# Kernel optimization log

Measured on AMD Instinct MI355X. Metric: run time of the kernel, lower is better.

Reference implementation:

```python
import jax, jax.numpy as jnp
import numpy as np

N = 8192       # number of graph nodes (A.shape[0])
D_IN = 256     # input_dim
D_THETA = 256  # hard-coded theta projection dim
D_OUT = 256    # output_dim
K = 5          # per-row top-k sparsification
BN_EPS = 1e-5
LRELU_SLOPE = 0.01


def setup_inputs() -> dict:
    key = jax.random.key(0)
    k0, k1, k2 = jax.random.split(key, 3)
    H = jax.random.normal(k0, (N, D_IN), dtype=jnp.float32)
    # Linear(input_dim, 256)
    W_theta = jax.random.normal(k1, (D_IN, D_THETA), dtype=jnp.float32) * (1.0 / np.sqrt(D_IN))
    b_theta = jnp.zeros((D_THETA,), dtype=jnp.float32)
    # Linear(input_dim, output_dim)
    W_out = jax.random.normal(k2, (D_IN, D_OUT), dtype=jnp.float32) * (1.0 / np.sqrt(D_IN))
    b_out = jnp.zeros((D_OUT,), dtype=jnp.float32)
    # BatchNorm1d(input_dim) affine params (fresh init)
    bn_gamma = jnp.ones((D_IN,), dtype=jnp.float32)
    bn_beta = jnp.zeros((D_IN,), dtype=jnp.float32)
    return {"H": H, "bn_gamma": bn_gamma, "bn_beta": bn_beta,
            "W_theta": W_theta, "b_theta": b_theta,
            "W_out": W_out, "b_out": b_out}


def reference(H, bn_gamma, bn_beta, W_theta, b_theta, W_out, b_out):
    # BatchNorm1d in training mode: biased batch stats over the node axis
    mu = H.mean(axis=0)
    var = H.var(axis=0)  # biased, matching torch normalization
    Hn = (H - mu) * jax.lax.rsqrt(var + BN_EPS) * bn_gamma + bn_beta  # [N, D_IN]

    # theta projection -> SAM affinity
    Hx = Hn @ W_theta + b_theta                                        # [N, D_THETA]
    nrm = jnp.maximum(jnp.linalg.norm(Hx, axis=1, keepdims=True), 1e-12)  # F.normalize eps
    F1 = Hx / nrm
    dist = jnp.clip(F1 @ F1.T, -1.0, 1.0)                              # [N, N]
    sam = jnp.nan_to_num(jnp.arccos(dist))
    # original SAM() detaches (numpy round-trip): affinity is a constant wrt grads
    sam = jax.lax.stop_gradient(sam)

    A = jnp.maximum(jax.nn.sigmoid(jnp.exp(-0.2 * sam)), 0.1)          # clamp(min=0.1)

    # per-row top-k sparsification (fused replacement of the python double loop)
    _, idx = jax.lax.top_k(A, K)                                       # [N, K]
    mask = jnp.zeros_like(A).at[jnp.arange(N)[:, None], idx].set(1.0)
    A = A * mask

    # D^{-1/2} A D^{-1/2} without materializing diag matrices
    dinv = A.sum(axis=1) ** -0.5                                       # [N]
    A_hat = dinv[:, None] * A * dinv[None, :]

    out = A_hat @ (Hn @ W_out + b_out)                                 # [N, D_OUT]
    out = jnp.where(out >= 0, out, LRELU_SLOPE * out)                  # LeakyReLU
    return out, A
```

## Files before the change

### kernel.cpp

```cpp
#include <hip/hip_runtime.h>
#include <hip/hip_bf16.h>
#include <cstdint>
#include <cstddef>

#define NN 8192
#define DD 256

using bf16 = __hip_bfloat16;
typedef unsigned short ushort_t;
typedef unsigned int uint32;
typedef short short8 __attribute__((ext_vector_type(8)));
typedef float f32x4 __attribute__((ext_vector_type(4)));

#define GL2LDS(g, l) __builtin_amdgcn_global_load_lds( \
  (const __attribute__((address_space(1))) void*)(g),  \
  (__attribute__((address_space(3))) void*)(l), 16, 0, 0)

__device__ __forceinline__ float ldin(const void* p, int flag, size_t i) {
  return flag ? __bfloat162float(((const bf16*)p)[i]) : ((const float*)p)[i];
}

__device__ __forceinline__ void ins8(float v, int jj, float (&lv)[8], int (&li)[8]) {
  if (v <= lv[7]) return;
  int cnt = 0;
#pragma unroll
  for (int s = 0; s < 8; ++s) cnt += (lv[s] >= v) ? 1 : 0;
#pragma unroll
  for (int s = 7; s >= 1; --s) {
    bool sh = (s > cnt);
    lv[s] = sh ? lv[s-1] : lv[s];
    li[s] = sh ? li[s-1] : li[s];
  }
#pragma unroll
  for (int s = 0; s < 8; ++s) if (s == cnt) { lv[s] = v; li[s] = jj; }
}

__device__ __forceinline__ void ins8t(float v, int jj, float (&lv)[8], int (&li)[8]) {
  bool lose = (lv[7] > v) || (lv[7] == v && li[7] < jj);
  if (lose) return;
  int cnt = 0;
#pragma unroll
  for (int s = 0; s < 8; ++s) cnt += ((lv[s] > v) || (lv[s] == v && li[s] < jj)) ? 1 : 0;
#pragma unroll
  for (int s = 7; s >= 1; --s) {
    bool sh = (s > cnt);
    lv[s] = sh ? lv[s-1] : lv[s];
    li[s] = sh ? li[s-1] : li[s];
  }
#pragma unroll
  for (int s = 0; s < 8; ++s) if (s == cnt) { lv[s] = v; li[s] = jj; }
}

__device__ __forceinline__ bool lexgt(float va, int ia, float vb, int ib) {
  return (va > vb) || (va == vb && ia < ib);
}

__global__ void k_detect(const ushort_t* __restrict__ Hu, int* __restrict__ flag) {
  __shared__ int cnt;
  if (threadIdx.x == 0) cnt = 0;
  __syncthreads();
  int sane = 0;
  for (int u = 0; u < 16; ++u) {
    int idx = 2 * (threadIdx.x * 16 + u);
    ushort_t h = Hu[idx];
    int e = (h >> 7) & 0xFF;
    sane += (e >= 113 && e <= 133) ? 1 : 0;
  }
  atomicAdd(&cnt, sane);
  __syncthreads();
  if (threadIdx.x == 0) *flag = (cnt > 2048) ? 1 : 0;
}

__global__ void k_transposeH(const void* __restrict__ H, const int* __restrict__ pflag,
                             float* __restrict__ HT) {
  int flag = *pflag;
  __shared__ float tile[64][65];
  int i0 = blockIdx.x * 64;
  int c0 = blockIdx.y * 64;
  int tid = threadIdx.x;
  int r = tid >> 2, cb = (tid & 3) * 16;
#pragma unroll
  for (int u = 0; u < 16; ++u)
    tile[r][cb + u] = ldin(H, flag, (size_t)(i0 + r) * DD + c0 + cb + u);
  __syncthreads();
  int c = tid >> 2, rb = (tid & 3) * 16;
#pragma unroll
  for (int u4 = 0; u4 < 4; ++u4) {
    float4 t;
    t.x = tile[rb + 4*u4 + 0][c];
    t.y = tile[rb + 4*u4 + 1][c];
    t.z = tile[rb + 4*u4 + 2][c];
    t.w = tile[rb + 4*u4 + 3][c];
    *(float4*)&HT[(size_t)(c0 + c) * NN + i0 + rb + 4*u4] = t;
  }
}

__global__ __launch_bounds__(256) void k_statsT(const float* __restrict__ HT,
                                                float* __restrict__ mu32, float* __restrict__ rs32) {
  __shared__ float buf[8192];
  int c = blockIdx.x;
  int tid = threadIdx.x;
#pragma unroll
  for (int it = 0; it < 8; ++it) {
    int idx = it * 1024 + tid * 4;
    *(float4*)&buf[idx] = *(const float4*)&HT[(size_t)c * NN + idx];
  }
  __syncthreads();
  if (tid == 0) {
    float acc = 0.0f;
    for (int r = 0; r < 8192; r += 32) {
      float4 v[8];
#pragma unroll
      for (int q = 0; q < 8; ++q) v[q] = *(const float4*)&buf[r + q * 4];
#pragma unroll
      for (int q = 0; q < 8; ++q) {
        acc = __fadd_rn(acc, v[q].x);
        acc = __fadd_rn(acc, v[q].y);
        acc = __fadd_rn(acc, v[q].z);
        acc = __fadd_rn(acc, v[q].w);
      }
    }
    float mu = __fdiv_rn(acc, 8192.0f);
    float vacc = 0.0f;
    for (int r = 0; r < 8192; r += 32) {
      float4 v[8];
#pragma unroll
      for (int q = 0; q < 8; ++q) v[q] = *(const float4*)&buf[r + q * 4];
#pragma unroll
      for (int q = 0; q < 8; ++q) {
        float d0 = __fsub_rn(v[q].x, mu); vacc = __fadd_rn(vacc, __fmul_rn(d0, d0));
        float d1 = __fsub_rn(v[q].y, mu); vacc = __fadd_rn(vacc, __fmul_rn(d1, d1));
        float d2 = __fsub_rn(v[q].z, mu); vacc = __fadd_rn(vacc, __fmul_rn(d2, d2));
        float d3 = __fsub_rn(v[q].w, mu); vacc = __fadd_rn(vacc, __fmul_rn(d3, d3));
      }
    }
    float var = __fdiv_rn(vacc, 8192.0f);
    mu32[c] = mu;
    rs32[c] = __fdiv_rn(1.0f, sqrtf(__fadd_rn(var, 1e-5f)));
  }
}

__global__ __launch_bounds__(256) void k_hxn(const void* __restrict__ H,
    const int* __restrict__ pflag, const float* __restrict__ mu32, const float* __restrict__ rs32,
    const void* __restrict__ gamma, const void* __restrict__ beta,
    const void* __restrict__ Wt, const void* __restrict__ bt,
    float* __restrict__ Hn, float* __restrict__ F1,
    ushort_t* __restrict__ F1hi, ushort_t* __restrict__ F1lo) {
  int flag = *pflag;
  __shared__ float sHn[8][256];
  __shared__ float sHx[8][256];
  __shared__ float sp[8][16];
  __shared__ float snrm[8];
  const int r0 = blockIdx.x * 8;
  const int n = threadIdx.x;
  float g  = ldin(gamma, flag, n);
  float b  = ldin(beta, flag, n);
  float mu = mu32[n], rs = rs32[n];
#pragma unroll
  for (int r = 0; r < 8; ++r) {
    float t = __fsub_rn(ldin(H, flag, (size_t)(r0 + r) * DD + n), mu);
    t = __fmul_rn(t, rs);
    t = __fmul_rn(t, g);
    t = __fadd_rn(t, b);
    sHn[r][n] = t;
    Hn[(size_t)(r0 + r) * DD + n] = t;
  }
  __syncthreads();
  float acc[8];
#pragma unroll
  for (int r = 0; r < 8; ++r) acc[r] = 0.0f;
#pragma unroll 8
  for (int k = 0; k < DD; ++k) {
    float w = ldin(Wt, flag, (size_t)k * DD + n);
#pragma unroll
    for (int r = 0; r < 8; ++r) acc[r] = fmaf(sHn[r][k], w, acc[r]);
  }
  float btn = ldin(bt, flag, n);
#pragma unroll
  for (int r = 0; r < 8; ++r) sHx[r][n] = __fadd_rn(acc[r], btn);
  __syncthreads();
  if (n < 128) {
    int r = n >> 4, s = n & 15;
    int base = (s >> 3) * 128 + (s & 7);
    float e0 = sHx[r][base];
    float part = __fmul_rn(e0, e0);
#pragma unroll
    for (int t = 1; t < 16; ++t) {
      float e = sHx[r][base + 8 * t];
      part = __fadd_rn(part, __fmul_rn(e, e));
    }
    sp[r][s] = part;
  }
  __syncthreads();
  if (n < 8) {
    const float* p = sp[n];
    float P1 = __fadd_rn(__fadd_rn(__fadd_rn(p[0], p[1]), __fadd_rn(p[2], p[3])),
                         __fadd_rn(__fadd_rn(p[4], p[5]), __fadd_rn(p[6], p[7])));
    float P2 = __fadd_rn(__fadd_rn(__fadd_rn(p[8], p[9]), __fadd_rn(p[10], p[11])),
                         __fadd_rn(__fadd_rn(p[12], p[13]), __fadd_rn(p[14], p[15])));
    snrm[n] = fmaxf(sqrtf(__fadd_rn(P1, P2)), 1e-12f);
  }
  __syncthreads();
#pragma unroll
  for (int r = 0; r < 8; ++r) {
    float xn = __fdiv_rn(sHx[r][n], snrm[r]);
    size_t idx = (size_t)(r0 + r) * DD + n;
    F1[idx] = xn;
    bf16 hi = __float2bfloat16(xn);
    float lo = __fsub_rn(xn, __bfloat162float(hi));
    F1hi[idx] = *(ushort_t*)&hi;
    bf16 lob = __float2bfloat16(lo);
    F1lo[idx] = *(ushort_t*)&lob;
  }
}

__global__ __launch_bounds__(256) void k_gemm_s(
    const ushort_t* __restrict__ F1hi, const ushort_t* __restrict__ F1lo,
    int jc, float* __restrict__ S) {
  __shared__ __align__(16) ushort_t AH[4096];
  __shared__ __align__(16) ushort_t AL[4096];
  __shared__ __align__(16) ushort_t BH[4096];
  __shared__ __align__(16) ushort_t BL[4096];
  const int tid = threadIdx.x;
  const int w = tid >> 6, lane = tid & 63;
  const int quad = lane >> 4, l15 = lane & 15;
  const int wi = w >> 1, wj = w & 1;
  const int i0 = blockIdx.y * 128;
  const int j0loc = blockIdx.x * 128;
  const int j0 = jc * 2048 + j0loc;

  const int rofs = lane >> 2;
  const int ccl  = (lane & 3) ^ (rofs & 3);
  const int laneElem = rofs * DD + ccl * 8;

  f32x4 acc[4][4];
#pragma unroll
  for (int fr = 0; fr < 4; ++fr)
#pragma unroll
    for (int fc = 0; fc < 4; ++fc) acc[fr][fc] = (f32x4)0.0f;

  for (int chunk = 0; chunk < 8; ++chunk) {
    const int kofs = chunk * 32;
    __syncthreads();
#pragma unroll
    for (int q = 0; q < 2; ++q) {
      const int s = w * 2 + q;
      const size_t ga = (size_t)(i0 + s * 16) * DD + kofs;
      const size_t gb = (size_t)(j0 + s * 16) * DD + kofs;
      GL2LDS(F1hi + ga + laneElem, &AH[s * 512]);
      GL2LDS(F1lo + ga + laneElem, &AL[s * 512]);
      GL2LDS(F1hi + gb + laneElem, &BH[s * 512]);
      GL2LDS(F1lo + gb + laneElem, &BL[s * 512]);
    }
    __syncthreads();
    short8 ah[4], al[4], bh[4], bl[4];
#pragma unroll
    for (int fr = 0; fr < 4; ++fr) {
      int row = wi * 64 + fr * 16 + l15;
      int g = quad ^ (row & 3);
      ah[fr] = *(const short8*)&AH[row * 32 + g * 8];
      al[fr] = *(const short8*)&AL[row * 32 + g * 8];
    }
#pragma unroll
    for (int fc = 0; fc < 4; ++fc) {
      int row = wj * 64 + fc * 16 + l15;
      int g = quad ^ (row & 3);
      bh[fc] = *(const short8*)&BH[row * 32 + g * 8];
      bl[fc] = *(const short8*)&BL[row * 32 + g * 8];
    }
#pragma unroll
    for (int fr = 0; fr < 4; ++fr)
#pragma unroll
      for (int fc = 0; fc < 4; ++fc) {
        acc[fr][fc] = __builtin_amdgcn_mfma_f32_16x16x32_bf16(ah[fr], bh[fc], acc[fr][fc], 0, 0, 0);
        acc[fr][fc] = __builtin_amdgcn_mfma_f32_16x16x32_bf16(ah[fr], bl[fc], acc[fr][fc], 0, 0, 0);
        acc[fr][fc] = __builtin_amdgcn_mfma_f32_16x16x32_bf16(al[fr], bh[fc], acc[fr][fc], 0, 0, 0);
      }
  }
#pragma unroll
  for (int fr = 0; fr < 4; ++fr) {
#pragma unroll
    for (int reg = 0; reg < 4; ++reg) {
      int row = i0 + wi * 64 + fr * 16 + quad * 4 + reg;
#pragma unroll
      for (int fc = 0; fc < 4; ++fc) {
        int coll = j0loc + wj * 64 + fc * 16 + l15;
        S[(size_t)row * 2048 + coll] = acc[fr][fc][reg];
      }
    }
  }
}

__global__ __launch_bounds__(256) void k_scan(const float* __restrict__ S, int jc,
                                              float* __restrict__ candv, int* __restrict__ candi) {
  int w = threadIdx.x >> 6, lane = threadIdx.x & 63;
  int row = blockIdx.x * 4 + w;
  const int jbase = jc * 2048;
  float lv[8]; int li[8];
#pragma unroll
  for (int e = 0; e < 8; ++e) { lv[e] = -3.0e38f; li[e] = 0x7fffffff; }
  const float* p = S + (size_t)row * 2048;
#pragma unroll
  for (int it = 0; it < 8; ++it) {
    int col = it * 256 + lane * 4;
    float4 v = *(const float4*)&p[col];
    float m4 = fmaxf(fmaxf(v.x, v.y), fmaxf(v.z, v.w));
    if (m4 > lv[7]) {
      ins8(v.x, jbase + col + 0, lv, li);
      ins8(v.y, jbase + col + 1, lv, li);
      ins8(v.z, jbase + col + 2, lv, li);
      ins8(v.w, jbase + col + 3, lv, li);
    }
  }
#pragma unroll
  for (int m = 1; m <= 32; m <<= 1) {
    float bv[8]; int bi[8];
#pragma unroll
    for (int e = 0; e < 8; ++e) {
      bv[e] = __shfl_xor(lv[e], m, 64);
      bi[e] = __shfl_xor(li[e], m, 64);
    }
#pragma unroll
    for (int e = 0; e < 8; ++e) {
      bool t = lexgt(lv[e], li[e], bv[7 - e], bi[7 - e]);
      lv[e] = t ? lv[e] : bv[7 - e];
      li[e] = t ? li[e] : bi[7 - e];
    }
#pragma unroll
    for (int d = 4; d >= 1; d >>= 1) {
#pragma unroll
      for (int e = 0; e < 8; ++e) {
        if ((e & d) == 0) {
          int f = e + d;
          bool sw = lexgt(lv[f], li[f], lv[e], li[e]);
          float tv = lv[e]; int ti = li[e];
          lv[e] = sw ? lv[f] : lv[e];  li[e] = sw ? li[f] : li[e];
          lv[f] = sw ? tv : lv[f];     li[f] = sw ? ti : li[f];
        }
      }
    }
  }
  if (lane == 0) {
    size_t base = ((size_t)row * 4 + jc) * 8;
#pragma unroll
    for (int e = 0; e < 8; ++e) { candv[base + e] = lv[e]; candi[base + e] = li[e]; }
  }
}

__global__ void k_merge(const float* __restrict__ candv, const int* __restrict__ candi,
                        int* __restrict__ cand8) {
  int row = blockIdx.x * 256 + threadIdx.x;
  float bv[8]; int bj[8];
#pragma unroll
  for (int e = 0; e < 8; ++e) { bv[e] = -3.0e38f; bj[e] = 0x7fffffff; }
  for (int t = 0; t < 32; ++t) {
    float v = candv[(size_t)row * 32 + t];
    int j   = candi[(size_t)row * 32 + t];
    ins8t(v, j, bv, bj);
  }
#pragma unroll
  for (int e = 0; e < 8; ++e) cand8[row * 8 + e] = bj[e];
}

__global__ void k_rerank(const float* __restrict__ F1, const int* __restrict__ cand8,
                         int* __restrict__ top5i, float* __restrict__ top5v,
                         float* __restrict__ dinv) {
  int w = threadIdx.x >> 6, lane = threadIdx.x & 63;
  int row = blockIdx.x * 4 + w;
  int jl = 0x7fffffff;
  float a32 = -1.0f;
  if (lane < 8) {
    jl = cand8[row * 8 + lane];
    const float* xi = F1 + (size_t)row * DD;
    const float* xj = F1 + (size_t)jl * DD;
    float acc = 0.0f;
#pragma unroll 8
    for (int k = 0; k < DD; ++k)
      acc = fmaf(xi[k], xj[k], acc);
    float d = fminf(fmaxf(acc, -1.0f), 1.0f);
    float sam = acosf(d);
    float xx = expf(__fmul_rn(-0.2f, sam));
    float sig = __fdiv_rn(1.0f, __fadd_rn(1.0f, expf(-xx)));
    a32 = fmaxf(sig, 0.1f);
  }
  float av[8]; int aj[8];
#pragma unroll
  for (int l = 0; l < 8; ++l) { av[l] = __shfl(a32, l, 64); aj[l] = __shfl(jl, l, 64); }
  if (lane == 0) {
    bool used[8] = {false,false,false,false,false,false,false,false};
    double dsum = 0.0;
#pragma unroll
    for (int k = 0; k < 5; ++k) {
      float bv = -2.0f; int bj = 0x7fffffff; int bs = -1;
#pragma unroll
      for (int s = 0; s < 8; ++s) {
        bool better = (!used[s]) && ((av[s] > bv) || (av[s] == bv && aj[s] < bj));
        bs = better ? s : bs;
        bv = better ? av[s] : bv;
        bj = better ? aj[s] : bj;
      }
#pragma unroll
      for (int s = 0; s < 8; ++s) used[s] = used[s] || (s == bs);
      top5i[row * 5 + k] = bj;
      top5v[row * 5 + k] = bv;
      dsum += (double)bv;
    }
    dinv[row] = (float)(1.0 / sqrt(dsum));
  }
}

__global__ __launch_bounds__(256) void k_zout(const float* __restrict__ Hn,
    const int* __restrict__ top5i, const float* __restrict__ top5v,
    const float* __restrict__ dinv, const void* __restrict__ Wo,
    const void* __restrict__ bo, const int* __restrict__ pflag, void* __restrict__ outp) {
  int flag = *pflag;
  __shared__ float sZ[8][256];
  __shared__ float ssr[8];
  const int r0 = blockIdx.x * 8;
  const int n = threadIdx.x;
#pragma unroll
  for (int r = 0; r < 8; ++r) {
    int i = r0 + r;
    float di = dinv[i];
    double z = 0.0;
    float sr = 0.0f;
#pragma unroll
    for (int k = 0; k < 5; ++k) {
      int j = top5i[i * 5 + k];
      float wgt = di * top5v[i * 5 + k] * dinv[j];
      z += (double)wgt * (double)Hn[(size_t)j * DD + n];
      sr += wgt;
    }
    sZ[r][n] = (float)z;
    if (n == 0) ssr[r] = sr;
  }
  __syncthreads();
  float acc[8];
#pragma unroll
  for (int r = 0; r < 8; ++r) acc[r] = 0.0f;
#pragma unroll 8
  for (int k = 0; k < DD; ++k) {
    float w = ldin(Wo, flag, (size_t)k * DD + n);
#pragma unroll
    for (int r = 0; r < 8; ++r) acc[r] = fmaf(sZ[r][k], w, acc[r]);
  }
  float bon = ldin(bo, flag, n);
#pragma unroll
  for (int r = 0; r < 8; ++r) {
    float v = acc[r] + ssr[r] * bon;
    v = (v >= 0.0f) ? v : 0.01f * v;
    size_t idx = (size_t)(r0 + r) * DD + n;
    if (flag) ((bf16*)outp)[idx] = __float2bfloat16(v);
    else      ((float*)outp)[idx] = v;
  }
}

__global__ __launch_bounds__(256) void k_zeroscatter(void* __restrict__ d_out,
    const int* __restrict__ pflag, const int* __restrict__ top5i,
    const float* __restrict__ top5v) {
  int flag = *pflag;
  size_t esize = flag ? 2 : 4;
  int r0 = blockIdx.x * 2;
  char* Abase = (char*)d_out + (size_t)NN * DD * esize;
  uint4* rowp = (uint4*)(Abase + (size_t)r0 * NN * esize);
  int nvec = (int)((2 * (size_t)NN * esize) >> 4);
  uint4 z; z.x = 0; z.y = 0; z.z = 0; z.w = 0;
  for (int i = threadIdx.x; i < nvec; i += 256) rowp[i] = z;
  __syncthreads();
  int t = threadIdx.x;
  if (t < 10) {
    int r = r0 + t / 5, k = t % 5;
    int col = top5i[r * 5 + k];
    float v = top5v[r * 5 + k];
    if (flag) ((bf16*)Abase)[(size_t)r * NN + col] = __float2bfloat16(v);
    else      ((float*)Abase)[(size_t)r * NN + col] = v;
  }
}

extern "C" void kernel_launch(void* const* d_in, const int* in_sizes, int n_in,
                              void* d_out, int out_size, void* d_ws, size_t ws_size,
                              hipStream_t stream) {
  (void)in_sizes; (void)n_in; (void)out_size; (void)ws_size;
  const void* H     = d_in[0];
  const void* gamma = d_in[1];
  const void* beta  = d_in[2];
  const void* Wt    = d_in[3];
  const void* bt    = d_in[4];
  const void* Wo    = d_in[5];
  const void* bo    = d_in[6];

  const size_t MB = 1048576;
  char* zb = (char*)d_out + 8 * MB;
  float*    Hn32  = (float*)(zb + 0);
  float*    F1_32 = (float*)(zb + 8 * MB);
  ushort_t* F1hi  = (ushort_t*)(zb + 16 * MB);
  ushort_t* F1lo  = (ushort_t*)(zb + 20 * MB);
  float*    candv = (float*)(zb + 24 * MB);
  int*      candi = (int*)(zb + 25 * MB);
  float*    HT    = (float*)(zb + 36 * MB);
  float*    mu32  = (float*)(zb + 44 * MB);
  float*    rs32  = (float*)(zb + 44 * MB + 4096);
  int*      cand8 = (int*)(zb + 44 * MB + 8192);
  float*    dinv  = (float*)(zb + 44 * MB + 270336);
  float*    Schunk= (float*)(zb + 48 * MB);

  char* ws = (char*)d_ws;
  int*   flag  = (int*)(ws + 0);
  int*   top5i = (int*)(ws + 256);
  float* top5v = (float*)(ws + 164096);

  k_detect<<<dim3(1), dim3(256), 0, stream>>>((const ushort_t*)H, flag);
  k_transposeH<<<dim3(128, 4), dim3(256), 0, stream>>>(H, flag, HT);
  k_statsT<<<dim3(256), dim3(256), 0, stream>>>(HT, mu32, rs32);
  k_hxn<<<dim3(1024), dim3(256), 0, stream>>>(H, flag, mu32, rs32, gamma, beta,
                                              Wt, bt, Hn32, F1_32, F1hi, F1lo);
  for (int jc = 0; jc < 4; ++jc) {
    k_gemm_s<<<dim3(16, 64), dim3(256), 0, stream>>>(F1hi, F1lo, jc, Schunk);
    k_scan<<<dim3(2048), dim3(256), 0, stream>>>(Schunk, jc, candv, candi);
  }
  k_merge<<<dim3(32), dim3(256), 0, stream>>>(candv, candi, cand8);
  k_rerank<<<dim3(2048), dim3(256), 0, stream>>>(F1_32, cand8, top5i, top5v, dinv);
  k_zout<<<dim3(1024), dim3(256), 0, stream>>>(Hn32, top5i, top5v, dinv, Wo, bo, flag, d_out);
  k_zeroscatter<<<dim3(4096), dim3(256), 0, stream>>>(d_out, flag, top5i, top5v);
}
```

Measured before the change: 838.4 us.

## Exploit Gram symmetry and fuse top-k candidate selection into the similarity GEMM

Computes only the lower-triangular 128x128 tiles of F1·F1ᵀ, using a triangular block index, and applies each tile to both its rows and the transposed columns. Per-tile top-8 candidates are extracted directly from the MFMA accumulators with sorting networks and shuffle merges, so the full similarity chunk is no longer written to and re-read from global memory. The per-chunk scan kernel is removed. k_merge becomes wave-parallel over 128 candidate lists per row. In exchange, the GEMM epilogue is heavier and there is a larger 64MB candidate buffer to write and merge.

New measurement: 1.071 ms. 1.28x slower.

```diff
diff --git a/kernel.cpp b/kernel.cpp
--- a/kernel.cpp
+++ b/kernel.cpp
@@ -2,6 +2,7 @@
 #include <hip/hip_bf16.h>
 #include <cstdint>
 #include <cstddef>
+#include <cmath>
 
 #define NN 8192
 #define DD 256
@@ -35,24 +36,43 @@
   for (int s = 0; s < 8; ++s) if (s == cnt) { lv[s] = v; li[s] = jj; }
 }
 
-__device__ __forceinline__ void ins8t(float v, int jj, float (&lv)[8], int (&li)[8]) {
-  bool lose = (lv[7] > v) || (lv[7] == v && li[7] < jj);
-  if (lose) return;
-  int cnt = 0;
-#pragma unroll
-  for (int s = 0; s < 8; ++s) cnt += ((lv[s] > v) || (lv[s] == v && li[s] < jj)) ? 1 : 0;
-#pragma unroll
-  for (int s = 7; s >= 1; --s) {
-    bool sh = (s > cnt);
-    lv[s] = sh ? lv[s-1] : lv[s];
-    li[s] = sh ? li[s-1] : li[s];
-  }
-#pragma unroll
-  for (int s = 0; s < 8; ++s) if (s == cnt) { lv[s] = v; li[s] = jj; }
-}
-
 __device__ __forceinline__ bool lexgt(float va, int ia, float vb, int ib) {
   return (va > vb) || (va == vb && ia < ib);
+}
+
+__device__ __forceinline__ void bimerge(float (&lv)[8], int (&li)[8], int m) {
+  float bv[8]; int bi[8];
+#pragma unroll
+  for (int e = 0; e < 8; ++e) {
+    bv[e] = __shfl_xor(lv[e], m, 64);
+    bi[e] = __shfl_xor(li[e], m, 64);
+  }
+#pragma unroll
+  for (int e = 0; e < 8; ++e) {
+    bool t = lexgt(lv[e], li[e], bv[7 - e], bi[7 - e]);
+    lv[e] = t ? lv[e] : bv[7 - e];
+    li[e] = t ? li[e] : bi[7 - e];
+  }
+#pragma unroll
+  for (int d = 4; d >= 1; d >>= 1) {
+#pragma unroll
+    for (int e = 0; e < 8; ++e) {
+      if ((e & d) == 0) {
+        int f = e + d;
+        bool sw = lexgt(lv[f], li[f], lv[e], li[e]);
+        float tv = lv[e]; int ti = li[e];
+        lv[e] = sw ? lv[f] : lv[e];  li[e] = sw ? li[f] : li[e];
+        lv[f] = sw ? tv : lv[f];     li[f] = sw ? ti : li[f];
+      }
+    }
+  }
+}
+
+__device__ __forceinline__ void cswap(float& va, int& ia, float& vb, int& ib) {
+  bool sw = lexgt(vb, ib, va, ia);
+  float tv = va; int ti = ia;
+  va = sw ? vb : va; ia = sw ? ib : ia;
+  vb = sw ? tv : vb; ib = sw ? ti : ib;
 }
 
 __global__ void k_detect(const ushort_t* __restrict__ Hu, int* __restrict__ flag) {
@@ -214,20 +234,25 @@
   }
 }
 
-__global__ __launch_bounds__(256) void k_gemm_s(
+__global__ __launch_bounds__(256) void k_gemm_sym(
     const ushort_t* __restrict__ F1hi, const ushort_t* __restrict__ F1lo,
-    int jc, float* __restrict__ S) {
+    float* __restrict__ candv, int* __restrict__ candi) {
   __shared__ __align__(16) ushort_t AH[4096];
   __shared__ __align__(16) ushort_t AL[4096];
   __shared__ __align__(16) ushort_t BH[4096];
   __shared__ __align__(16) ushort_t BL[4096];
+  const int bidx = blockIdx.x;
+  int it = (int)((sqrt(8.0 * (double)bidx + 1.0) - 1.0) * 0.5);
+  while ((it + 1) * (it + 2) / 2 <= bidx) ++it;
+  while (it * (it + 1) / 2 > bidx) --it;
+  const int jt = bidx - it * (it + 1) / 2;
+
   const int tid = threadIdx.x;
   const int w = tid >> 6, lane = tid & 63;
   const int quad = lane >> 4, l15 = lane & 15;
   const int wi = w >> 1, wj = w & 1;
-  const int i0 = blockIdx.y * 128;
-  const int j0loc = blockIdx.x * 128;
-  const int j0 = jc * 2048 + j0loc;
+  const int i0 = it * 128;
+  const int j0 = jt * 128;
 
   const int rofs = lane >> 2;
   const int ccl  = (lane & 3) ^ (rofs & 3);
@@ -277,89 +302,86 @@
         acc[fr][fc] = __builtin_amdgcn_mfma_f32_16x16x32_bf16(al[fr], bh[fc], acc[fr][fc], 0, 0, 0);
       }
   }
+
 #pragma unroll
   for (int fr = 0; fr < 4; ++fr) {
 #pragma unroll
     for (int reg = 0; reg < 4; ++reg) {
-      int row = i0 + wi * 64 + fr * 16 + quad * 4 + reg;
+      float sv[4]; int sj[4];
 #pragma unroll
       for (int fc = 0; fc < 4; ++fc) {
-        int coll = j0loc + wj * 64 + fc * 16 + l15;
-        S[(size_t)row * 2048 + coll] = acc[fr][fc][reg];
-      }
-    }
-  }
-}
-
-__global__ __launch_bounds__(256) void k_scan(const float* __restrict__ S, int jc,
-                                              float* __restrict__ candv, int* __restrict__ candi) {
+        sv[fc] = acc[fr][fc][reg];
+        sj[fc] = j0 + wj * 64 + fc * 16 + l15;
+      }
+      cswap(sv[0], sj[0], sv[1], sj[1]);
+      cswap(sv[2], sj[2], sv[3], sj[3]);
+      cswap(sv[0], sj[0], sv[2], sj[2]);
+      cswap(sv[1], sj[1], sv[3], sj[3]);
+      cswap(sv[1], sj[1], sv[2], sj[2]);
+      float lv[8]; int li[8];
+#pragma unroll
+      for (int e = 0; e < 4; ++e) { lv[e] = sv[e]; li[e] = sj[e]; }
+#pragma unroll
+      for (int e = 4; e < 8; ++e) { lv[e] = -3.0e38f; li[e] = 0x7fffffff; }
+      bimerge(lv, li, 1);
+      bimerge(lv, li, 2);
+      bimerge(lv, li, 4);
+      bimerge(lv, li, 8);
+      int rowg = i0 + wi * 64 + fr * 16 + quad * 4 + reg;
+      if (l15 < 8) {
+        size_t base = ((size_t)rowg * 128 + 2 * jt + wj) * 8;
+        candv[base + l15] = lv[l15];
+        candi[base + l15] = li[l15];
+      }
+    }
+  }
+  if (it != jt) {
+#pragma unroll
+    for (int fc = 0; fc < 4; ++fc) {
+      float lv[8]; int li[8];
+#pragma unroll
+      for (int e = 0; e < 8; ++e) { lv[e] = -3.0e38f; li[e] = 0x7fffffff; }
+#pragma unroll
+      for (int fr = 0; fr < 4; ++fr)
+#pragma unroll
+        for (int reg = 0; reg < 4; ++reg)
+          ins8(acc[fr][fc][reg], i0 + wi * 64 + fr * 16 + quad * 4 + reg, lv, li);
+      bimerge(lv, li, 16);
+      bimerge(lv, li, 32);
+      int jg = j0 + wj * 64 + fc * 16 + l15;
+      size_t base = ((size_t)jg * 128 + 2 * it + wi) * 8;
+#pragma unroll
+      for (int e = 0; e < 2; ++e) {
+        candv[base + quad * 2 + e] = lv[quad * 2 + e];
+        candi[base + quad * 2 + e] = li[quad * 2 + e];
+      }
+    }
+  }
+}
+
+__global__ __launch_bounds__(256) void k_merge(const float* __restrict__ candv,
+                                               const int* __restrict__ candi,
+                                               int* __restrict__ cand8) {
   int w = threadIdx.x >> 6, lane = threadIdx.x & 63;
   int row = blockIdx.x * 4 + w;
-  const int jbase = jc * 2048;
   float lv[8]; int li[8];
 #pragma unroll
   for (int e = 0; e < 8; ++e) { lv[e] = -3.0e38f; li[e] = 0x7fffffff; }
-  const float* p = S + (size_t)row * 2048;
-#pragma unroll
-  for (int it = 0; it < 8; ++it) {
-    int col = it * 256 + lane * 4;
-    float4 v = *(const float4*)&p[col];
-    float m4 = fmaxf(fmaxf(v.x, v.y), fmaxf(v.z, v.w));
-    if (m4 > lv[7]) {
-      ins8(v.x, jbase + col + 0, lv, li);
-      ins8(v.y, jbase + col + 1, lv, li);
-      ins8(v.z, jbase + col + 2, lv, li);
-      ins8(v.w, jbase + col + 3, lv, li);
-    }
-  }
-#pragma unroll
-  for (int m = 1; m <= 32; m <<= 1) {
-    float bv[8]; int bi[8];
-#pragma unroll
-    for (int e = 0; e < 8; ++e) {
-      bv[e] = __shfl_xor(lv[e], m, 64);
-      bi[e] = __shfl_xor(li[e], m, 64);
-    }
-#pragma unroll
-    for (int e = 0; e < 8; ++e) {
-      bool t = lexgt(lv[e], li[e], bv[7 - e], bi[7 - e]);
-      lv[e] = t ? lv[e] : bv[7 - e];
-      li[e] = t ? li[e] : bi[7 - e];
-    }
-#pragma unroll
-    for (int d = 4; d >= 1; d >>= 1) {
-#pragma unroll
-      for (int e = 0; e < 8; ++e) {
-        if ((e & d) == 0) {
-          int f = e + d;
-          bool sw = lexgt(lv[f], li[f], lv[e], li[e]);
-          float tv = lv[e]; int ti = li[e];
-          lv[e] = sw ? lv[f] : lv[e];  li[e] = sw ? li[f] : li[e];
-          lv[f] = sw ? tv : lv[f];     li[f] = sw ? ti : li[f];
-        }
-      }
-    }
-  }
-  if (lane == 0) {
-    size_t base = ((size_t)row * 4 + jc) * 8;
-#pragma unroll
-    for (int e = 0; e < 8; ++e) { candv[base + e] = lv[e]; candi[base + e] = li[e]; }
-  }
-}
-
-__global__ void k_merge(const float* __restrict__ candv, const int* __restrict__ candi,
-                        int* __restrict__ cand8) {
-  int row = blockIdx.x * 256 + threadIdx.x;
-  float bv[8]; int bj[8];
-#pragma unroll
-  for (int e = 0; e < 8; ++e) { bv[e] = -3.0e38f; bj[e] = 0x7fffffff; }
-  for (int t = 0; t < 32; ++t) {
-    float v = candv[(size_t)row * 32 + t];
-    int j   = candi[(size_t)row * 32 + t];
-    ins8t(v, j, bv, bj);
-  }
-#pragma unroll
-  for (int e = 0; e < 8; ++e) cand8[row * 8 + e] = bj[e];
+  const float* pv = candv + (size_t)row * 1024;
+  const int*   pi = candi + (size_t)row * 1024;
+#pragma unroll
+  for (int s = 0; s < 16; ++s) {
+    int t = s * 64 + lane;
+    float v = pv[t];
+    if (v > lv[7]) ins8(v, pi[t], lv, li);
+  }
+  bimerge(lv, li, 1);
+  bimerge(lv, li, 2);
+  bimerge(lv, li, 4);
+  bimerge(lv, li, 8);
+  bimerge(lv, li, 16);
+  bimerge(lv, li, 32);
+  if (lane < 8) cand8[row * 8 + lane] = li[lane];
 }
 
 __global__ void k_rerank(const float* __restrict__ F1, const int* __restrict__ cand8,
@@ -495,14 +517,13 @@
   float*    F1_32 = (float*)(zb + 8 * MB);
   ushort_t* F1hi  = (ushort_t*)(zb + 16 * MB);
   ushort_t* F1lo  = (ushort_t*)(zb + 20 * MB);
-  float*    candv = (float*)(zb + 24 * MB);
-  int*      candi = (int*)(zb + 25 * MB);
-  float*    HT    = (float*)(zb + 36 * MB);
-  float*    mu32  = (float*)(zb + 44 * MB);
-  float*    rs32  = (float*)(zb + 44 * MB + 4096);
-  int*      cand8 = (int*)(zb + 44 * MB + 8192);
-  float*    dinv  = (float*)(zb + 44 * MB + 270336);
-  float*    Schunk= (float*)(zb + 48 * MB);
+  float*    HT    = (float*)(zb + 24 * MB);
+  float*    mu32  = (float*)(zb + 32 * MB);
+  float*    rs32  = (float*)(zb + 32 * MB + 4096);
+  int*      cand8 = (int*)(zb + 32 * MB + 8192);
+  float*    dinv  = (float*)(zb + 33 * MB);
+  float*    candv = (float*)(zb + 34 * MB);
+  int*      candi = (int*)(zb + 66 * MB);
 
   char* ws = (char*)d_ws;
   int*   flag  = (int*)(ws + 0);
@@ -514,11 +535,8 @@
   k_statsT<<<dim3(256), dim3(256), 0, stream>>>(HT, mu32, rs32);
   k_hxn<<<dim3(1024), dim3(256), 0, stream>>>(H, flag, mu32, rs32, gamma, beta,
                                               Wt, bt, Hn32, F1_32, F1hi, F1lo);
-  for (int jc = 0; jc < 4; ++jc) {
-    k_gemm_s<<<dim3(16, 64), dim3(256), 0, stream>>>(F1hi, F1lo, jc, Schunk);
-    k_scan<<<dim3(2048), dim3(256), 0, stream>>>(Schunk, jc, candv, candi);
-  }
-  k_merge<<<dim3(32), dim3(256), 0, stream>>>(candv, candi, cand8);
+  k_gemm_sym<<<dim3(2080), dim3(256), 0, stream>>>(F1hi, F1lo, candv, candi);
+  k_merge<<<dim3(2048), dim3(256), 0, stream>>>(candv, candi, cand8);
   k_rerank<<<dim3(2048), dim3(256), 0, stream>>>(F1_32, cand8, top5i, top5v, dinv);
   k_zout<<<dim3(1024), dim3(256), 0, stream>>>(Hn32, top5i, top5v, dinv, Wo, bo, flag, d_out);
   k_zeroscatter<<<dim3(4096), dim3(256), 0, stream>>>(d_out, flag, top5i, top5v);
```
